# Kernel tuning notes

Hardware: AMD Instinct MI355X
Metric: run time of the kernel (lower is better)

Reference implementation:

```python
import jax, jax.numpy as jnp
import numpy as np

# MLS-MPM constants (init_kwargs)
N_GRID = 128
DT = 2e-4
DX = 1.0 / N_GRID
INV_DX = float(N_GRID)
P_VOL = (DX * 0.5) ** 3
P_RHO = 1000.0
P_MASS = P_VOL * P_RHO
GRAVITY = 9.8
BOUND = 3
N_PART = 500_000

# 27 neighbor offsets for quadratic B-spline stencil
_OFFS = np.stack(np.meshgrid(np.arange(3), np.arange(3), np.arange(3), indexing='ij'), -1).reshape(27, 3)


def setup_inputs() -> dict:
    key = jax.random.key(0)
    k1, k2, k3, k4, k5 = jax.random.split(key, 5)
    # particles strictly inside the domain, away from boundary cells
    x = 0.2 + 0.6 * jax.random.uniform(k1, (N_PART, 3), dtype=jnp.float32)
    v = 0.1 * jax.random.normal(k2, (N_PART, 3), dtype=jnp.float32)
    C = 0.1 * jax.random.normal(k3, (N_PART, 3, 3), dtype=jnp.float32)
    F = jnp.eye(3, dtype=jnp.float32) + 0.01 * jax.random.normal(k4, (N_PART, 3, 3), dtype=jnp.float32)
    stress = 1e2 * jax.random.normal(k5, (N_PART, 3, 3), dtype=jnp.float32)
    return {"x": x, "v": v, "C": C, "F": F, "stress": stress}


def _mpm_step(x, v, C, F, stress):
    dtype = x.dtype
    base = jnp.floor(x * INV_DX - 0.5).astype(jnp.int32)          # [N,3]
    fx = x * INV_DX - base.astype(dtype)                          # [N,3] in [0.5, 1.5)
    # quadratic B-spline weights per node offset (0,1,2) per axis: [N,3off,3ax]
    w = jnp.stack([0.5 * (1.5 - fx) ** 2,
                   0.75 - (fx - 1.0) ** 2,
                   0.5 * (fx - 0.5) ** 2], axis=1)
    offs = jnp.asarray(_OFFS, dtype=jnp.int32)                    # [27,3]
    weight = w[:, offs[:, 0], 0] * w[:, offs[:, 1], 1] * w[:, offs[:, 2], 2]  # [N,27]
    dpos = (offs[None].astype(dtype) - fx[:, None, :]) * DX       # [N,27,3] world units

    # P2G scatter: momentum (3) + mass (1) per grid node
    affine = (-DT * P_VOL * 4.0 * INV_DX * INV_DX) * stress + P_MASS * C   # [N,3,3]
    mv = P_MASS * v[:, None, :] + jnp.einsum('nij,nkj->nki', affine, dpos) # [N,27,3]
    vals = jnp.concatenate([weight[..., None] * mv,
                            (weight * P_MASS)[..., None]], axis=-1)        # [N,27,4]
    node = jnp.clip(base[:, None, :] + offs[None], 0, N_GRID - 1)          # [N,27,3]
    flat = (node[..., 0] * N_GRID + node[..., 1]) * N_GRID + node[..., 2]  # [N,27]
    grid = jnp.zeros((N_GRID ** 3, 4), dtype).at[flat.reshape(-1)].add(vals.reshape(-1, 4))

    # grid update: normalize momentum, gravity, sticky boundary
    gm = grid[:, 3:4]
    occ = gm[:, 0] > 0
    gv = jnp.where(gm > 0, grid[:, :3] / jnp.maximum(gm, 1e-10), 0.0)
    gv = gv.at[:, 1].add(jnp.where(occ, jnp.asarray(-DT * GRAVITY, dtype), 0.0))
    gv3 = gv.reshape(N_GRID, N_GRID, N_GRID, 3)
    idx = jnp.arange(N_GRID)
    for axis in range(3):  # fixed 3-axis loop (not a data loop)
        shp = [1, 1, 1]; shp[axis] = N_GRID
        lo = (idx < BOUND).reshape(shp)
        hi = (idx >= N_GRID - BOUND).reshape(shp)
        comp = gv3[..., axis]
        comp = jnp.where(lo & (comp < 0), 0.0, comp)
        comp = jnp.where(hi & (comp > 0), 0.0, comp)
        gv3 = gv3.at[..., axis].set(comp)
    gvf = gv3.reshape(-1, 3)

    # G2P gather
    gvp = gvf[flat]                                               # [N,27,3]
    v_next = jnp.einsum('nk,nkd->nd', weight, gvp)
    C_next = (4.0 * INV_DX * INV_DX) * jnp.einsum('nk,nki,nkj->nij', weight, gvp, dpos)
    x_next = x + DT * v_next
    F_next = jnp.einsum('nij,njk->nik', jnp.eye(3, dtype=dtype) + DT * C_next, F)
    return x_next, v_next, C_next, F_next


def reference(x, v, C, F, stress):
    return _mpm_step(x, v, C, F, stress)
```

## Files before the change

kernel.cpp:

```cpp
#include <hip/hip_runtime.h>
#include <limits.h>

#define N_GRID 128
#define N_GRID3 (N_GRID * N_GRID * N_GRID)

constexpr int   N_PART   = 500000;
constexpr float DT       = 0.0002f;
constexpr float DX       = 1.0f / 128.0f;
constexpr float INV_DX   = 128.0f;
constexpr float P_MASS   = 5.9604644775390625e-05f;
constexpr float AFF_COEF = -7.8125e-07f;
constexpr float GRAVITY  = 9.8f;
constexpr int   BOUND    = 3;
constexpr float C_SCALE  = 65536.0f;
constexpr int   ZQ       = 2;

__global__ __launch_bounds__(256) void k_count(const float* __restrict__ x,
                                               int* __restrict__ cnt,
                                               int* __restrict__ blkMin,
                                               int* __restrict__ blkMax) {
  __shared__ int lmin[12], lmax[12];
  int n = blockIdx.x * 256 + threadIdx.x;
  int bx = INT_MAX, by = INT_MAX, bz = INT_MAX;
  int mx = -1, my = -1, mz = -1;
  if (n < N_PART) {
    bx = min(max((int)floorf(x[n * 3 + 0] * INV_DX - 0.5f), 0), N_GRID - 1);
    by = min(max((int)floorf(x[n * 3 + 1] * INV_DX - 0.5f), 0), N_GRID - 1);
    bz = min(max((int)floorf(x[n * 3 + 2] * INV_DX - 0.5f), 0), N_GRID - 1);
    int c = (bx << 14) | (by << 7) | bz;
    atomicAdd(&cnt[c], 1);
    mx = bx; my = by; mz = bz;
  }
#pragma unroll
  for (int d = 32; d > 0; d >>= 1) {
    bx = min(bx, __shfl_xor(bx, d));
    by = min(by, __shfl_xor(by, d));
    bz = min(bz, __shfl_xor(bz, d));
    mx = max(mx, __shfl_xor(mx, d));
    my = max(my, __shfl_xor(my, d));
    mz = max(mz, __shfl_xor(mz, d));
  }
  int lane = threadIdx.x & 63, wid = threadIdx.x >> 6;
  if (lane == 0) {
    lmin[wid * 3 + 0] = bx; lmin[wid * 3 + 1] = by; lmin[wid * 3 + 2] = bz;
    lmax[wid * 3 + 0] = mx; lmax[wid * 3 + 1] = my; lmax[wid * 3 + 2] = mz;
  }
  __syncthreads();
  if (threadIdx.x == 0) {
    int b = blockIdx.x;
#pragma unroll
    for (int a = 0; a < 3; ++a) {
      blkMin[b * 3 + a] = min(min(lmin[a], lmin[3 + a]), min(lmin[6 + a], lmin[9 + a]));
      blkMax[b * 3 + a] = max(max(lmax[a], lmax[3 + a]), max(lmax[6 + a], lmax[9 + a]));
    }
  }
}

__global__ __launch_bounds__(256) void k_scan1(const int* __restrict__ cnt,
                                               int* __restrict__ blkSum) {
  __shared__ int ws[4];
  int tid = threadIdx.x, lane = tid & 63, wid = tid >> 6;
  int4 v = ((const int4*)cnt)[blockIdx.x * 256 + tid];
  int s = v.x + v.y + v.z + v.w;
  for (int d = 32; d > 0; d >>= 1) s += __shfl_down(s, d);
  if (lane == 0) ws[wid] = s;
  __syncthreads();
  if (tid == 0) blkSum[blockIdx.x] = ws[0] + ws[1] + ws[2] + ws[3];
}

__global__ __launch_bounds__(256) void k_scan2(const int* __restrict__ blkSum,
                                               int* __restrict__ blkOff,
                                               int* __restrict__ start,
                                               const int* __restrict__ blkMin,
                                               const int* __restrict__ blkMax,
                                               int nblkP,
                                               int* __restrict__ bbox) {
  __shared__ int wsum[4];
  __shared__ int rmin[12], rmax[12];
  int tid = threadIdx.x, lane = tid & 63, wid = tid >> 6;

  int base = tid * 8;
  int s[8], tot = 0;
#pragma unroll
  for (int j = 0; j < 8; ++j) { s[j] = blkSum[base + j]; tot += s[j]; }
  int incl = tot;
  for (int d = 1; d < 64; d <<= 1) {
    int t = __shfl_up(incl, d);
    if (lane >= d) incl += t;
  }
  if (lane == 63) wsum[wid] = incl;
  __syncthreads();
  int woff = 0;
  for (int w = 0; w < wid; ++w) woff += wsum[w];
  int run = woff + incl - tot;
#pragma unroll
  for (int j = 0; j < 8; ++j) { blkOff[base + j] = run; run += s[j]; }
  if (tid == 255) start[N_GRID3] = run;

  int bx = INT_MAX, by = INT_MAX, bz = INT_MAX;
  int mx = -1, my = -1, mz = -1;
  for (int j = tid; j < nblkP; j += 256) {
    bx = min(bx, blkMin[j * 3 + 0]);
    by = min(by, blkMin[j * 3 + 1]);
    bz = min(bz, blkMin[j * 3 + 2]);
    mx = max(mx, blkMax[j * 3 + 0]);
    my = max(my, blkMax[j * 3 + 1]);
    mz = max(mz, blkMax[j * 3 + 2]);
  }
#pragma unroll
  for (int d = 32; d > 0; d >>= 1) {
    bx = min(bx, __shfl_xor(bx, d));
    by = min(by, __shfl_xor(by, d));
    bz = min(bz, __shfl_xor(bz, d));
    mx = max(mx, __shfl_xor(mx, d));
    my = max(my, __shfl_xor(my, d));
    mz = max(mz, __shfl_xor(mz, d));
  }
  if (lane == 0) {
    rmin[wid * 3 + 0] = bx; rmin[wid * 3 + 1] = by; rmin[wid * 3 + 2] = bz;
    rmax[wid * 3 + 0] = mx; rmax[wid * 3 + 1] = my; rmax[wid * 3 + 2] = mz;
  }
  __syncthreads();
  if (tid == 0) {
#pragma unroll
    for (int a = 0; a < 3; ++a) {
      bbox[a]     = min(min(rmin[a], rmin[3 + a]), min(rmin[6 + a], rmin[9 + a]));
      bbox[3 + a] = max(max(rmax[a], rmax[3 + a]), max(rmax[6 + a], rmax[9 + a]));
    }
  }
}

__global__ __launch_bounds__(256) void k_scan3(int* __restrict__ cnt,
                                               const int* __restrict__ blkOff,
                                               int* __restrict__ start) {
  __shared__ int wsum[4];
  int tid = threadIdx.x, lane = tid & 63, wid = tid >> 6;
  int b = blockIdx.x;
  int4 v = ((const int4*)cnt)[b * 256 + tid];
  int s = v.x + v.y + v.z + v.w;
  int incl = s;
  for (int d = 1; d < 64; d <<= 1) {
    int t = __shfl_up(incl, d);
    if (lane >= d) incl += t;
  }
  if (lane == 63) wsum[wid] = incl;
  __syncthreads();
  int woff = blkOff[b];
  for (int w = 0; w < wid; ++w) woff += wsum[w];
  int run = woff + incl - s;
  int i0 = (b * 256 + tid) * 4;
  int r0 = run, r1 = r0 + v.x, r2 = r1 + v.y, r3 = r2 + v.z;
  start[i0 + 0] = r0; start[i0 + 1] = r1; start[i0 + 2] = r2; start[i0 + 3] = r3;
  cnt[i0 + 0] = r0; cnt[i0 + 1] = r1; cnt[i0 + 2] = r2; cnt[i0 + 3] = r3;
}

__global__ __launch_bounds__(256) void k_reorder(
    const float* __restrict__ x, const float* __restrict__ v,
    const float* __restrict__ C, const float* __restrict__ S,
    const float* __restrict__ F,
    int* __restrict__ cursor, float4* __restrict__ posO,
    float4* __restrict__ aux, float* __restrict__ fs) {
  int n = blockIdx.x * 256 + threadIdx.x;
  if (n >= N_PART) return;

  float px = x[n * 3 + 0], py = x[n * 3 + 1], pz = x[n * 3 + 2];
  int bx = min(max((int)floorf(px * INV_DX - 0.5f), 0), N_GRID - 1);
  int by = min(max((int)floorf(py * INV_DX - 0.5f), 0), N_GRID - 1);
  int bz = min(max((int)floorf(pz * INV_DX - 0.5f), 0), N_GRID - 1);
  int c = (bx << 14) | (by << 7) | bz;
  int pos = atomicAdd(&cursor[c], 1);

  float mvx = P_MASS * v[n * 3 + 0];
  float mvy = P_MASS * v[n * 3 + 1];
  float mvz = P_MASS * v[n * 3 + 2];
  float aff[9];
#pragma unroll
  for (int k = 0; k < 9; ++k)
    aff[k] = AFF_COEF * S[n * 9 + k] + P_MASS * C[n * 9 + k];

  posO[pos] = make_float4(px, py, pz, __int_as_float(n));
  float4* dst = aux + (size_t)pos * 3;
  dst[0] = make_float4(mvx, mvy, mvz, aff[0]);
  dst[1] = make_float4(aff[1], aff[2], aff[3], aff[4]);
  dst[2] = make_float4(aff[5], aff[6], aff[7], aff[8]);

  if (fs) {
#pragma unroll
    for (int k = 0; k < 9; ++k) fs[(size_t)pos * 9 + k] = F[(size_t)n * 9 + k];
  }
}

__device__ __forceinline__ float wq(int o, float f) {
  if (o == 0) return 0.5f * (1.5f - f) * (1.5f - f);
  if (o == 1) return 0.75f - (f - 1.0f) * (f - 1.0f);
  return 0.5f * (f - 0.5f) * (f - 0.5f);
}

__global__ __launch_bounds__(256) void mpm_p2g(
    const int* __restrict__ start, const float4* __restrict__ posO,
    const float4* __restrict__ aux, const int* __restrict__ bbox,
    float* __restrict__ grid ) {
  int bx0 = bbox[0], by0 = bbox[1], bz0c = bbox[2];
  int nxd = bbox[3] - bx0 + 3;
  int nyd = bbox[4] - by0 + 3;
  int nzd = bbox[5] - bz0c + 3;
  int dimzq = (nzd + ZQ - 1) / ZQ;
  int vol = nxd * nyd * dimzq;
  int nact = (vol + 255) >> 8;

  int bid = blockIdx.x;
  if (bid >= nact) return;
  int q = nact >> 3, r = nact & 7;
  int xcd = bid & 7, sub = bid >> 3;
  int wgid = (xcd < r ? xcd * (q + 1) : r * (q + 1) + (xcd - r) * q) + sub;

  int t = wgid * 256 + (int)threadIdx.x;
  if (t >= vol) return;
  int izq = t % dimzq;
  int rr = t / dimzq;
  int iy = rr % nyd;
  int ix = rr / nyd;
  int nx = bx0 + ix, ny = by0 + iy, nz0 = bz0c + izq * ZQ;
  if (nx > N_GRID - 1 || ny > N_GRID - 1) return;
  int zb0 = nz0 - 2;
  bool zint = (zb0 >= 0) && (zb0 + ZQ + 2 <= N_GRID);

  float accx[ZQ], accy[ZQ], accz[ZQ], accm[ZQ];
#pragma unroll
  for (int k = 0; k < ZQ; ++k) { accx[k] = 0.f; accy[k] = 0.f; accz[k] = 0.f; accm[k] = 0.f; }
  int gotmask = 0;

#pragma unroll
  for (int dy = -2; dy <= 0; ++dy) {
    int cy = ny + dy;
    if (cy < 0) continue;
#pragma unroll
    for (int dx = -2; dx <= 0; ++dx) {
      int cx = nx + dx;
      if (cx < 0) continue;
      const int ox = -dx, oy = -dy;
      int rowb = (cx << 14) | (cy << 7);

      int S[ZQ + 3];
      if (zint) {
#pragma unroll
        for (int j = 0; j < ZQ + 3; ++j) S[j] = start[rowb + zb0 + j];
      } else {
#pragma unroll
        for (int j = 0; j < ZQ + 3; ++j)
          S[j] = start[rowb + min(max(zb0 + j, 0), N_GRID)];
      }
#pragma unroll
      for (int k = 0; k < ZQ; ++k)
        gotmask |= (S[k + 3] > S[k]) ? (1 << k) : 0;

      for (int i = S[0]; i < S[ZQ + 2]; ++i) {
        float4 q0 = posO[i];
        const float4* ap = aux + (size_t)i * 3;
        float4 A0 = ap[0], A1 = ap[1], A2 = ap[2];

        float fx = q0.x * INV_DX - (float)cx;
        float fy = q0.y * INV_DX - (float)cy;
        float gz = q0.z * INV_DX;
        float bzf = floorf(gz - 0.5f);
        float fz = gz - bzf;
        int oz0 = nz0 - (int)bzf;

        float wxy = wq(ox, fx) * wq(oy, fy);
        float dpx = ((float)ox - fx) * DX;
        float dpy = ((float)oy - fy) * DX;
        float wz0 = 0.5f * (1.5f - fz) * (1.5f - fz);
        float wz1 = 0.75f - (fz - 1.0f) * (fz - 1.0f);
        float wz2 = 0.5f * (fz - 0.5f) * (fz - 0.5f);

        float sx = A0.x + A0.w * dpx + A1.x * dpy;
        float sy = A0.y + A1.z * dpx + A1.w * dpy;
        float sz = A0.z + A2.y * dpx + A2.z * dpy;
        float wm = wxy * P_MASS;

#pragma unroll
        for (int k = 0; k < ZQ; ++k) {
          int oz = oz0 + k;
          if (oz < 0 || oz > 2) continue;
          float wzz = (oz == 0) ? wz0 : ((oz == 1) ? wz1 : wz2);
          float w = wxy * wzz;
          float dpz = ((float)oz - fz) * DX;
          accx[k] += w * (sx + A1.y * dpz);
          accy[k] += w * (sy + A2.x * dpz);
          accz[k] += w * (sz + A2.w * dpz);
          accm[k] += wzz * wm;
        }
      }
    }
  }

  if (!gotmask) return;

  float4* g4 = (float4*)grid;
#pragma unroll
  for (int k = 0; k < ZQ; ++k) {
    int nz = nz0 + k;
    if (!((gotmask >> k) & 1) || nz > N_GRID - 1) continue;
    float m = accm[k];
    float ovx = 0.0f, ovy = 0.0f, ovz = 0.0f;
    if (m > 0.0f) {
      float inv = 1.0f / fmaxf(m, 1e-10f);
      ovx = accx[k] * inv;
      ovy = accy[k] * inv;
      ovz = accz[k] * inv;
      ovy -= DT * GRAVITY;
    }
    if (nx < BOUND && ovx < 0.0f) ovx = 0.0f;
    if (nx >= N_GRID - BOUND && ovx > 0.0f) ovx = 0.0f;
    if (ny < BOUND && ovy < 0.0f) ovy = 0.0f;
    if (ny >= N_GRID - BOUND && ovy > 0.0f) ovy = 0.0f;
    if (nz < BOUND && ovz < 0.0f) ovz = 0.0f;
    if (nz >= N_GRID - BOUND && ovz > 0.0f) ovz = 0.0f;
    g4[(nx << 14) | (ny << 7) | nz] = make_float4(ovx, ovy, ovz, m);
  }
}

__global__ __launch_bounds__(256) void mpm_g2p(
    const float4* __restrict__ posO, const float* __restrict__ F,
    const float* __restrict__ fs, const float* __restrict__ grid,
    float* __restrict__ out_x, float* __restrict__ out_v,
    float* __restrict__ out_C, float* __restrict__ out_F) {
  int i = blockIdx.x * blockDim.x + threadIdx.x;
  if (i >= N_PART) return;

  float4 q0 = posO[i];
  int n = __float_as_int(q0.w);

  float Fl[9];
  if (fs) {
#pragma unroll
    for (int k = 0; k < 9; ++k) Fl[k] = fs[(size_t)i * 9 + k];
  } else {
#pragma unroll
    for (int k = 0; k < 9; ++k) Fl[k] = F[(size_t)n * 9 + k];
  }

  float px = q0.x, py = q0.y, pz = q0.z;
  float gx = px * INV_DX, gy = py * INV_DX, gz = pz * INV_DX;
  int bx = (int)floorf(gx - 0.5f);
  int by = (int)floorf(gy - 0.5f);
  int bz = (int)floorf(gz - 0.5f);
  float fx = gx - (float)bx, fy = gy - (float)by, fz = gz - (float)bz;

  float wx[3], wy[3], wz[3];
  wx[0] = 0.5f * (1.5f - fx) * (1.5f - fx);
  wx[1] = 0.75f - (fx - 1.0f) * (fx - 1.0f);
  wx[2] = 0.5f * (fx - 0.5f) * (fx - 0.5f);
  wy[0] = 0.5f * (1.5f - fy) * (1.5f - fy);
  wy[1] = 0.75f - (fy - 1.0f) * (fy - 1.0f);
  wy[2] = 0.5f * (fy - 0.5f) * (fy - 0.5f);
  wz[0] = 0.5f * (1.5f - fz) * (1.5f - fz);
  wz[1] = 0.75f - (fz - 1.0f) * (fz - 1.0f);
  wz[2] = 0.5f * (fz - 0.5f) * (fz - 0.5f);

  float vnx = 0.0f, vny = 0.0f, vnz = 0.0f;
  float Cn[9];
#pragma unroll
  for (int k = 0; k < 9; ++k) Cn[k] = 0.0f;

  const float4* g4 = (const float4*)grid;
  bool interior = (bx >= 0) & (by >= 0) & (bz >= 0) &
                  (bx + 2 < N_GRID) & (by + 2 < N_GRID) & (bz + 2 < N_GRID);

  if (interior) {
    int flat0 = (bx << 14) | (by << 7) | bz;
#pragma unroll
    for (int a = 0; a < 3; ++a) {
#pragma unroll
      for (int bb = 0; bb < 3; ++bb) {
#pragma unroll
        for (int c = 0; c < 3; ++c) {
          float weight = wx[a] * wy[bb] * wz[c];
          float dpx = ((float)a - fx) * DX;
          float dpy = ((float)bb - fy) * DX;
          float dpz = ((float)c - fz) * DX;
          float4 g = g4[flat0 + (a << 14) + (bb << 7) + c];
          vnx += weight * g.x;
          vny += weight * g.y;
          vnz += weight * g.z;
          Cn[0] += weight * g.x * dpx;
          Cn[1] += weight * g.x * dpy;
          Cn[2] += weight * g.x * dpz;
          Cn[3] += weight * g.y * dpx;
          Cn[4] += weight * g.y * dpy;
          Cn[5] += weight * g.y * dpz;
          Cn[6] += weight * g.z * dpx;
          Cn[7] += weight * g.z * dpy;
          Cn[8] += weight * g.z * dpz;
        }
      }
    }
  } else {
#pragma unroll
    for (int a = 0; a < 3; ++a) {
#pragma unroll
      for (int bb = 0; bb < 3; ++bb) {
#pragma unroll
        for (int c = 0; c < 3; ++c) {
          float weight = wx[a] * wy[bb] * wz[c];
          float dpx = ((float)a - fx) * DX;
          float dpy = ((float)bb - fy) * DX;
          float dpz = ((float)c - fz) * DX;
          int nxg = min(max(bx + a, 0), N_GRID - 1);
          int nyg = min(max(by + bb, 0), N_GRID - 1);
          int nzg = min(max(bz + c, 0), N_GRID - 1);
          float4 g = g4[(nxg << 14) | (nyg << 7) | nzg];
          vnx += weight * g.x;
          vny += weight * g.y;
          vnz += weight * g.z;
          Cn[0] += weight * g.x * dpx;
          Cn[1] += weight * g.x * dpy;
          Cn[2] += weight * g.x * dpz;
          Cn[3] += weight * g.y * dpx;
          Cn[4] += weight * g.y * dpy;
          Cn[5] += weight * g.y * dpz;
          Cn[6] += weight * g.z * dpx;
          Cn[7] += weight * g.z * dpy;
          Cn[8] += weight * g.z * dpz;
        }
      }
    }
  }

#pragma unroll
  for (int k = 0; k < 9; ++k) Cn[k] *= C_SCALE;

  out_x[n * 3 + 0] = px + DT * vnx;
  out_x[n * 3 + 1] = py + DT * vny;
  out_x[n * 3 + 2] = pz + DT * vnz;
  out_v[n * 3 + 0] = vnx;
  out_v[n * 3 + 1] = vny;
  out_v[n * 3 + 2] = vnz;

  float A[9];
#pragma unroll
  for (int k = 0; k < 9; ++k) A[k] = DT * Cn[k];
  A[0] += 1.0f; A[4] += 1.0f; A[8] += 1.0f;

#pragma unroll
  for (int r = 0; r < 3; ++r) {
#pragma unroll
    for (int k = 0; k < 3; ++k) {
      float s = A[r * 3 + 0] * Fl[0 * 3 + k] +
                A[r * 3 + 1] * Fl[1 * 3 + k] +
                A[r * 3 + 2] * Fl[2 * 3 + k];
      out_F[n * 9 + r * 3 + k] = s;
    }
  }

#pragma unroll
  for (int k = 0; k < 9; ++k) out_C[n * 9 + k] = Cn[k];
}

extern "C" void kernel_launch(void* const* d_in, const int* in_sizes, int n_in,
                              void* d_out, int out_size, void* d_ws, size_t ws_size,
                              hipStream_t stream) {
  const float* x      = (const float*)d_in[0];
  const float* v      = (const float*)d_in[1];
  const float* C      = (const float*)d_in[2];
  const float* F      = (const float*)d_in[3];
  const float* stress = (const float*)d_in[4];

  float* out = (float*)d_out;
  char*  ws  = (char*)d_ws;

  const size_t GRID_BYTES  = (size_t)N_GRID3 * 4 * sizeof(float);
  const size_t POSO_BYTES  = (size_t)N_PART * sizeof(float4);
  const size_t AUX_BYTES   = (size_t)N_PART * 3 * sizeof(float4);
  const size_t CNT_BYTES   = (size_t)N_GRID3 * sizeof(int);
  const size_t START_BYTES = ((size_t)N_GRID3 + 1) * sizeof(int);
  const size_t FS_BYTES    = (size_t)N_PART * 9 * sizeof(float);

  int pblocks = (N_PART + 255) / 256;

  size_t off = 0;
  float*  grid   = (float*)(ws + off);  off += GRID_BYTES;
  float4* posO   = (float4*)(ws + off); off += POSO_BYTES;
  float4* aux    = (float4*)(ws + off); off += AUX_BYTES;
  int*    cnt    = (int*)(ws + off);    off += CNT_BYTES;
  int*    startp = (int*)(ws + off);    off += START_BYTES;
  int*    blkSum = (int*)(ws + off);    off += 2048 * sizeof(int);
  int*    blkOff = (int*)(ws + off);    off += 2048 * sizeof(int);
  int*    blkMin = (int*)(ws + off);    off += (size_t)pblocks * 3 * sizeof(int);
  int*    blkMax = (int*)(ws + off);    off += (size_t)pblocks * 3 * sizeof(int);
  int*    bbox   = (int*)(ws + off);    off += 16 * sizeof(int);
  off = (off + 255) & ~(size_t)255;
  float*  fs = (ws_size >= off + FS_BYTES) ? (float*)(ws + off) : nullptr;

  hipMemsetAsync(cnt, 0, CNT_BYTES, stream);

  k_count<<<pblocks, 256, 0, stream>>>(x, cnt, blkMin, blkMax);
  k_scan1<<<2048, 256, 0, stream>>>(cnt, blkSum);
  k_scan2<<<1, 256, 0, stream>>>(blkSum, blkOff, startp, blkMin, blkMax, pblocks, bbox);
  k_scan3<<<2048, 256, 0, stream>>>(cnt, blkOff, startp);
  k_reorder<<<pblocks, 256, 0, stream>>>(x, v, C, stress, F, cnt, posO, aux, fs);

  mpm_p2g<<<(N_GRID3 / ZQ + 255) / 256, 256, 0, stream>>>(startp, posO, aux, bbox, grid);

  float* out_x = out;
  float* out_v = out + (size_t)N_PART * 3;
  float* out_C = out + (size_t)N_PART * 6;
  float* out_F = out + (size_t)N_PART * 6 + (size_t)N_PART * 9;
  mpm_g2p<<<pblocks, 256, 0, stream>>>(posO, F, fs, grid, out_x, out_v, out_C, out_F);
}
```

Baseline: 203.5 us.

## Move F update into separate coalesced kernel reading C output

Removes the sorted copy of F that k_reorder wrote and g2p read back, and drops the F multiply from g2p. A new kernel k_ffinal runs in original particle order, reads the freshly written C and the input F with coalesced accesses, and writes the new F. This avoids one scattered read and one write of a 9-float-per-particle array, and it eases register pressure in g2p. In exchange it adds a kernel launch and re-reads C from global memory.

```diff
diff --git a/kernel.cpp b/kernel.cpp
--- a/kernel.cpp
+++ b/kernel.cpp
@@ -157,9 +157,8 @@
 __global__ __launch_bounds__(256) void k_reorder(
     const float* __restrict__ x, const float* __restrict__ v,
     const float* __restrict__ C, const float* __restrict__ S,
-    const float* __restrict__ F,
     int* __restrict__ cursor, float4* __restrict__ posO,
-    float4* __restrict__ aux, float* __restrict__ fs) {
+    float4* __restrict__ aux) {
   int n = blockIdx.x * 256 + threadIdx.x;
   if (n >= N_PART) return;
 
@@ -183,11 +182,6 @@
   dst[0] = make_float4(mvx, mvy, mvz, aff[0]);
   dst[1] = make_float4(aff[1], aff[2], aff[3], aff[4]);
   dst[2] = make_float4(aff[5], aff[6], aff[7], aff[8]);
-
-  if (fs) {
-#pragma unroll
-    for (int k = 0; k < 9; ++k) fs[(size_t)pos * 9 + k] = F[(size_t)n * 9 + k];
-  }
 }
 
 __device__ __forceinline__ float wq(int o, float f) {
@@ -321,24 +315,14 @@
 }
 
 __global__ __launch_bounds__(256) void mpm_g2p(
-    const float4* __restrict__ posO, const float* __restrict__ F,
-    const float* __restrict__ fs, const float* __restrict__ grid,
+    const float4* __restrict__ posO, const float* __restrict__ grid,
     float* __restrict__ out_x, float* __restrict__ out_v,
-    float* __restrict__ out_C, float* __restrict__ out_F) {
+    float* __restrict__ out_C) {
   int i = blockIdx.x * blockDim.x + threadIdx.x;
   if (i >= N_PART) return;
 
   float4 q0 = posO[i];
   int n = __float_as_int(q0.w);
-
-  float Fl[9];
-  if (fs) {
-#pragma unroll
-    for (int k = 0; k < 9; ++k) Fl[k] = fs[(size_t)i * 9 + k];
-  } else {
-#pragma unroll
-    for (int k = 0; k < 9; ++k) Fl[k] = F[(size_t)n * 9 + k];
-  }
 
   float px = q0.x, py = q0.y, pz = q0.z;
   float gx = px * INV_DX, gy = py * INV_DX, gz = pz * INV_DX;
@@ -436,11 +420,24 @@
   out_v[n * 3 + 0] = vnx;
   out_v[n * 3 + 1] = vny;
   out_v[n * 3 + 2] = vnz;
+#pragma unroll
+  for (int k = 0; k < 9; ++k) out_C[n * 9 + k] = Cn[k];
+}
+
+__global__ __launch_bounds__(256) void k_ffinal(
+    const float* __restrict__ out_C, const float* __restrict__ F,
+    float* __restrict__ out_F) {
+  int n = blockIdx.x * blockDim.x + threadIdx.x;
+  if (n >= N_PART) return;
 
   float A[9];
 #pragma unroll
-  for (int k = 0; k < 9; ++k) A[k] = DT * Cn[k];
+  for (int k = 0; k < 9; ++k) A[k] = DT * out_C[(size_t)n * 9 + k];
   A[0] += 1.0f; A[4] += 1.0f; A[8] += 1.0f;
+
+  float Fl[9];
+#pragma unroll
+  for (int k = 0; k < 9; ++k) Fl[k] = F[(size_t)n * 9 + k];
 
 #pragma unroll
   for (int r = 0; r < 3; ++r) {
@@ -449,12 +446,9 @@
       float s = A[r * 3 + 0] * Fl[0 * 3 + k] +
                 A[r * 3 + 1] * Fl[1 * 3 + k] +
                 A[r * 3 + 2] * Fl[2 * 3 + k];
-      out_F[n * 9 + r * 3 + k] = s;
-    }
-  }
-
-#pragma unroll
-  for (int k = 0; k < 9; ++k) out_C[n * 9 + k] = Cn[k];
+      out_F[(size_t)n * 9 + r * 3 + k] = s;
+    }
+  }
 }
 
 extern "C" void kernel_launch(void* const* d_in, const int* in_sizes, int n_in,
@@ -474,7 +468,6 @@
   const size_t AUX_BYTES   = (size_t)N_PART * 3 * sizeof(float4);
   const size_t CNT_BYTES   = (size_t)N_GRID3 * sizeof(int);
   const size_t START_BYTES = ((size_t)N_GRID3 + 1) * sizeof(int);
-  const size_t FS_BYTES    = (size_t)N_PART * 9 * sizeof(float);
 
   int pblocks = (N_PART + 255) / 256;
 
@@ -489,8 +482,6 @@
   int*    blkMin = (int*)(ws + off);    off += (size_t)pblocks * 3 * sizeof(int);
   int*    blkMax = (int*)(ws + off);    off += (size_t)pblocks * 3 * sizeof(int);
   int*    bbox   = (int*)(ws + off);    off += 16 * sizeof(int);
-  off = (off + 255) & ~(size_t)255;
-  float*  fs = (ws_size >= off + FS_BYTES) ? (float*)(ws + off) : nullptr;
 
   hipMemsetAsync(cnt, 0, CNT_BYTES, stream);
 
@@ -498,7 +489,7 @@
   k_scan1<<<2048, 256, 0, stream>>>(cnt, blkSum);
   k_scan2<<<1, 256, 0, stream>>>(blkSum, blkOff, startp, blkMin, blkMax, pblocks, bbox);
   k_scan3<<<2048, 256, 0, stream>>>(cnt, blkOff, startp);
-  k_reorder<<<pblocks, 256, 0, stream>>>(x, v, C, stress, F, cnt, posO, aux, fs);
+  k_reorder<<<pblocks, 256, 0, stream>>>(x, v, C, stress, cnt, posO, aux);
 
   mpm_p2g<<<(N_GRID3 / ZQ + 255) / 256, 256, 0, stream>>>(startp, posO, aux, bbox, grid);
 
@@ -506,5 +497,6 @@
   float* out_v = out + (size_t)N_PART * 3;
   float* out_C = out + (size_t)N_PART * 6;
   float* out_F = out + (size_t)N_PART * 6 + (size_t)N_PART * 9;
-  mpm_g2p<<<pblocks, 256, 0, stream>>>(posO, F, fs, grid, out_x, out_v, out_C, out_F);
-}
+  mpm_g2p<<<pblocks, 256, 0, stream>>>(posO, grid, out_x, out_v, out_C);
+  k_ffinal<<<pblocks, 256, 0, stream>>>(out_C, F, out_F);
+}
```

After: 189.7 us (median of 2 runs). 1.07x faster.
